# Kernel optimization log

Hardware: AMD Instinct MI355X
Metric: run time of the kernel (lower is better)

Reference implementation:

```python
import jax, jax.numpy as jnp
import numpy as np

NUM_HEADS = 16


def rotate_half(x):
    h = x.shape[-1] // 2
    return jnp.concatenate([-x[..., h:], x[..., :h]], axis=-1)


def setup_inputs() -> dict:
    key = jax.random.key(0)
    ks = jax.random.split(key, 8)
    S, dim, hd = 8192, 1280, 80
    n_seg = 8
    hidden_states = jax.random.normal(ks[0], (S, dim), dtype=jnp.float32)
    cu_seqlens = (jnp.arange(n_seg + 1, dtype=jnp.int32) * (S // n_seg))
    ang = jax.random.uniform(ks[1], (S, hd), dtype=jnp.float32) * (2.0 * np.pi)
    cos = jnp.cos(ang)
    sin = jnp.sin(ang)
    qkv_w = jax.random.normal(ks[2], (3 * dim, dim), dtype=jnp.float32) * (dim ** -0.5)
    qkv_b = jax.random.normal(ks[3], (3 * dim,), dtype=jnp.float32) * 0.02
    proj_w = jax.random.normal(ks[4], (dim, dim), dtype=jnp.float32) * (dim ** -0.5)
    proj_b = jax.random.normal(ks[5], (dim,), dtype=jnp.float32) * 0.02
    return {"hidden_states": hidden_states, "cu_seqlens": cu_seqlens,
            "cos": cos, "sin": sin, "qkv_w": qkv_w, "qkv_b": qkv_b,
            "proj_w": proj_w, "proj_b": proj_b}


def reference(hidden_states, cu_seqlens, cos, sin, qkv_w, qkv_b, proj_w, proj_b):
    S, dim = hidden_states.shape
    H = NUM_HEADS
    hd = dim // H
    scaling = hd ** -0.5

    # qkv projection: [S, 3*dim] -> [S, 3, H, hd]
    qkv = (hidden_states @ qkv_w.T + qkv_b).reshape(S, 3, H, hd)
    q, k, v = qkv[:, 0], qkv[:, 1], qkv[:, 2]  # each [S, H, hd]

    # RoPE in float32, cos/sin broadcast over heads
    c = cos[:, None, :].astype(jnp.float32)
    s = sin[:, None, :].astype(jnp.float32)
    qf, kf = q.astype(jnp.float32), k.astype(jnp.float32)
    q = (qf * c + rotate_half(qf) * s).astype(q.dtype)
    k = (kf * c + rotate_half(kf) * s).astype(k.dtype)

    # Block-diagonal varlen attention: equal-length segments -> batch dim
    lengths = np.diff(np.asarray(cu_seqlens))
    L = int(lengths[0])
    assert (lengths == L).all(), "reference assumes uniform segment lengths"
    B = lengths.shape[0]
    qb = q.reshape(B, L, H, hd)
    kb = k.reshape(B, L, H, hd)
    vb = v.reshape(B, L, H, hd)

    scores = jnp.einsum('blhd,bmhd->bhlm', qb, kb) * scaling
    probs = jax.nn.softmax(scores.astype(jnp.float32), axis=-1).astype(scores.dtype)
    out = jnp.einsum('bhlm,bmhd->blhd', probs, vb).reshape(S, dim)

    return out @ proj_w.T + proj_b
```

## Files before the change

### kernel.cpp

```cpp
#include <hip/hip_runtime.h>
#include <math.h>

typedef _Float16 f16;
typedef _Float16 half8 __attribute__((ext_vector_type(8)));
typedef _Float16 half4v __attribute__((ext_vector_type(4)));
typedef _Float16 half2v __attribute__((ext_vector_type(2)));
typedef float floatx4 __attribute__((ext_vector_type(4)));
typedef unsigned int u32;

#define AS1 __attribute__((address_space(1)))
#define AS3 __attribute__((address_space(3)))

__device__ __forceinline__ void stage16(f16* l, const f16* g) {
    __builtin_amdgcn_global_load_lds((const AS1 u32*)g, (AS3 u32*)l, 16, 0, 0);
}

__global__ __launch_bounds__(256) void cvt_f32_f16(const float* __restrict__ in,
                                                   f16* __restrict__ out, int n4) {
    int i = blockIdx.x * blockDim.x + threadIdx.x;
    if (i >= n4) return;
    float4 v = ((const float4*)in)[i];
    half4v h = {(f16)v.x, (f16)v.y, (f16)v.z, (f16)v.w};
    ((half4v*)out)[i] = h;
}

__global__ __launch_bounds__(256) void pack_w(const float* __restrict__ Wf,
                                              f16* __restrict__ Wp) {
    const int p = blockIdx.x * 256 + threadIdx.x;
    const int lane = p & 63;
    const int j = (p >> 6) & 3;
    const int sk = p >> 8;
    const int k0 = sk % 40;
    const int slab = sk / 40;
    const int row = slab * 64 + j * 16 + (lane & 15);
    const int col = k0 * 32 + (lane >> 4) * 8;
    const float* src = Wf + (size_t)row * 1280 + col;
    float4 a = *(const float4*)src;
    float4 b = *(const float4*)(src + 4);
    half8 h = {(f16)a.x, (f16)a.y, (f16)a.z, (f16)a.w,
               (f16)b.x, (f16)b.y, (f16)b.z, (f16)b.w};
    *(half8*)(Wp + (size_t)p * 8) = h;
}

constexpr int GK = 1280;
constexpr int KT = 20;

template <int MT>
__global__ __launch_bounds__(512, 2) void gemm_bp(const f16* __restrict__ A,
                                                  const f16* __restrict__ Bp,
                                                  const float* __restrict__ bias,
                                                  f16* __restrict__ outH,
                                                  float* __restrict__ outF,
                                                  int N, int NT) {
    constexpr int M_FR = MT / 32;
    constexpr int QE = MT * 32;
    __shared__ f16 sm[2][2][QE];
    const int t = threadIdx.x;
    const int lane = t & 63, w = t >> 6;
    const int wm = w >> 2, wn = w & 3;
    const int c16 = lane & 15, quad = lane >> 4;
    const int id = blockIdx.x;
    const int nx = (int)gridDim.x >> 3;
    const int gid = (id & 7) * nx + (id >> 3);
    const int bm = gid / NT, bn = gid - bm * NT;
    const f16* Ab = A + (size_t)bm * MT * GK;
    const f16* Bw = Bp + (size_t)(bn * 4 + wn) * (40 * 4 * 64 * 8) + lane * 8;

    floatx4 acc[M_FR][4] = {};
    half8 bfA[8], bfB[8];

    auto stageA = [&](int kt, int dst) {
#pragma unroll
        for (int ks = 0; ks < 2; ks++)
#pragma unroll
            for (int u = 0; u < MT / 128; u++) {
                const int c = t + u * 512;
                const int row = c >> 2;
                const int lc = ((c & 3) - (row >> 1)) & 3;
                stage16(&sm[dst][ks][0] + c * 8,
                        Ab + (size_t)row * GK + kt * 64 + ks * 32 + lc * 8);
            }
    };
    auto loadB = [&](int kt, half8(&bf)[8]) {
#pragma unroll
        for (int ks = 0; ks < 2; ks++)
#pragma unroll
            for (int j = 0; j < 4; j++)
                bf[ks * 4 + j] = *(const half8*)(Bw + (size_t)((kt * 2 + ks) * 4 + j) * 512);
    };
    auto compute = [&](int p, half8(&bf)[8]) {
#pragma unroll
        for (int ks = 0; ks < 2; ks++) {
            const f16* q = &sm[p][ks][0];
#pragma unroll
            for (int m = 0; m < M_FR; m++) {
                const int r = wm * (MT / 2) + m * 16 + c16;
                half8 a = *(const half8*)(q + r * 32 + (((quad + (r >> 1)) & 3) * 8));
#pragma unroll
                for (int n = 0; n < 4; n++)
                    acc[m][n] = __builtin_amdgcn_mfma_f32_16x16x32_f16(a, bf[ks * 4 + n],
                                                                       acc[m][n], 0, 0, 0);
            }
        }
    };
#define WAIT_STEADY()                                              \
    if constexpr (MT == 256) {                                     \
        asm volatile("s_waitcnt vmcnt(12)" ::: "memory");          \
    } else {                                                       \
        asm volatile("s_waitcnt vmcnt(10)" ::: "memory");          \
    }

    stageA(0, 0);
    loadB(0, bfA);
    asm volatile("s_waitcnt vmcnt(8)" ::: "memory");
    __builtin_amdgcn_s_barrier();

    for (int i = 0; i < 10; i++) {
        const int k0 = 2 * i;
        asm volatile("s_waitcnt lgkmcnt(0)" ::: "memory");
        __builtin_amdgcn_s_barrier();
        stageA(k0 + 1, 1);
        loadB(k0 + 1, bfB);
        WAIT_STEADY();
        __builtin_amdgcn_s_barrier();
        compute(0, bfA);
        asm volatile("s_waitcnt lgkmcnt(0)" ::: "memory");
        __builtin_amdgcn_s_barrier();
        if (i < 9) {
            stageA(k0 + 2, 0);
            loadB(k0 + 2, bfA);
            WAIT_STEADY();
        } else {
            asm volatile("s_waitcnt vmcnt(0)" ::: "memory");
        }
        __builtin_amdgcn_s_barrier();
        compute(1, bfB);
    }

    const int colBase = bn * 256 + wn * 64;
    const size_t rowBase = (size_t)bm * MT + wm * (MT / 2);
    float bv[4];
#pragma unroll
    for (int n = 0; n < 4; n++) bv[n] = bias[colBase + n * 16 + c16];
#pragma unroll
    for (int m = 0; m < M_FR; m++) {
#pragma unroll
        for (int r = 0; r < 4; r++) {
            const size_t row = rowBase + m * 16 + quad * 4 + r;
#pragma unroll
            for (int n = 0; n < 4; n++) {
                const int col = colBase + n * 16 + c16;
                const float v = acc[m][n][r] + bv[n];
                if (outH) outH[row * (size_t)N + col] = (f16)v;
                else      outF[row * (size_t)N + col] = v;
            }
        }
    }
}

#define QSCALE (0.11180339887498949f * 1.4426950408889634f)

__global__ __launch_bounds__(320) void rope_kernel(const f16* __restrict__ qkv,
                                                   const float* __restrict__ cosp,
                                                   const float* __restrict__ sinp,
                                                   f16* __restrict__ qb, f16* __restrict__ kb,
                                                   f16* __restrict__ vt) {
    constexpr int S = 8192;
    const int bs = blockIdx.x, h = blockIdx.y, t = threadIdx.x;
    const int sl = t / 5, g = t % 5;
    const int s = bs * 64 + sl;
    {
        const size_t base = (size_t)s * 3840 + h * 80 + g * 8;
        half8 qa = *(const half8*)(qkv + base);
        half8 qc = *(const half8*)(qkv + base + 40);
        half8 ka = *(const half8*)(qkv + base + 1280);
        half8 kc = *(const half8*)(qkv + base + 1320);
        const float* cp = cosp + (size_t)s * 80 + g * 8;
        const float* sp = sinp + (size_t)s * 80 + g * 8;
        half8 qo0, qo1, ko0, ko1;
#pragma unroll
        for (int j = 0; j < 8; j++) {
            float c0 = cp[j], c1 = cp[j + 40];
            float n0 = sp[j], n1 = sp[j + 40];
            float q0 = (float)qa[j], q1 = (float)qc[j];
            float k0 = (float)ka[j], k1 = (float)kc[j];
            qo0[j] = (f16)((q0 * c0 - q1 * n0) * QSCALE);
            qo1[j] = (f16)((q1 * c1 + q0 * n1) * QSCALE);
            ko0[j] = (f16)(k0 * c0 - k1 * n0);
            ko1[j] = (f16)(k1 * c1 + k0 * n1);
        }
        const size_t ob = ((size_t)h * S + s) * 96 + g * 8;
        *(half8*)(qb + ob)      = qo0;
        *(half8*)(qb + ob + 40) = qo1;
        *(half8*)(kb + ob)      = ko0;
        *(half8*)(kb + ob + 40) = ko1;
        if (g < 2) {
            half8 qp = {}, kp = {};
            if (g == 0) { qp[0] = (f16)(-8.0f); kp[0] = (f16)(1.0f); }
            const size_t pb = ((size_t)h * S + s) * 96 + 80 + g * 8;
            *(half8*)(qb + pb) = qp;
            *(half8*)(kb + pb) = kp;
        }
    }
    __shared__ f16 vls[64][81];
    for (int j = t; j < 64 * 80; j += 320) {
        int s2 = j / 80, d = j % 80;
        vls[s2][d] = qkv[((size_t)(bs * 64 + s2)) * 3840 + 2560 + h * 80 + d];
    }
    __syncthreads();
    for (int j = t; j < 64 * 80; j += 320) {
        int d = j >> 6, s2 = j & 63;
        vt[((size_t)(h * 80 + d)) * S + bs * 64 + s2] = vls[s2][d];
    }
}

__global__ __launch_bounds__(256, 2) void attn_kernel(const f16* __restrict__ qb,
                                                      const f16* __restrict__ kb,
                                                      const f16* __restrict__ vt,
                                                      const int* __restrict__ cu,
                                                      f16* __restrict__ out) {
    constexpr int S = 8192;
    __shared__ f16 Ks[2][64 * 96];
    __shared__ f16 Ps[256 * 72];
    const int t = threadIdx.x, lane = t & 63, w = t >> 6;
    const int c16 = lane & 15, quad = lane >> 4;
    const int id = blockIdx.x;
    const int pair = id & 127;
    const int qt = id >> 7;
    const int h = pair & 15, z = pair >> 4;
    const int s0 = cu[z];

    half8 qf[4][3];
#pragma unroll
    for (int qt2 = 0; qt2 < 4; qt2++)
#pragma unroll
        for (int ks = 0; ks < 3; ks++)
            qf[qt2][ks] = *(const half8*)(qb + ((size_t)h * S + s0 + qt * 256 + w * 64 + qt2 * 16 + c16) * 96 + ks * 32 + quad * 8);

    const f16 ov = (c16 == 0) ? (f16)1.f : (f16)0.f;
    const half8 onesf = {ov, ov, ov, ov, ov, ov, ov, ov};

    const int sR = t >> 2;
    const int sK = ((t & 3) - (sR >> 1)) & 3;

    {
        const f16* Kg = kb + ((size_t)h * S + s0) * 96;
#pragma unroll
        for (int j = 0; j < 3; j++)
            stage16(&Ks[0][0] + (j * 256 + t) * 8, Kg + (size_t)sR * 96 + j * 32 + sK * 8);
    }
    __syncthreads();

    floatx4 o[6][4] = {};

    for (int kv = 0; kv < 16; kv++) {
        if (kv < 15) {
            const f16* Kg = kb + ((size_t)h * S + s0 + (kv + 1) * 64) * 96;
            f16* Kd = &Ks[(kv + 1) & 1][0];
#pragma unroll
            for (int j = 0; j < 3; j++)
                stage16(Kd + (j * 256 + t) * 8, Kg + (size_t)sR * 96 + j * 32 + sK * 8);
        }
        const f16* Kc = &Ks[kv & 1][0];
        floatx4 sc[4][4] = {};
#pragma unroll
        for (int ks = 0; ks < 3; ks++) {
            half8 kf[4];
#pragma unroll
            for (int mt = 0; mt < 4; mt++) {
                const int row = mt * 16 + c16;
                kf[mt] = *(const half8*)(Kc + (ks * 256 + 4 * row + ((quad + (row >> 1)) & 3)) * 8);
            }
#pragma unroll
            for (int qt2 = 0; qt2 < 4; qt2++)
#pragma unroll
                for (int mt = 0; mt < 4; mt++)
                    sc[mt][qt2] = __builtin_amdgcn_mfma_f32_16x16x32_f16(kf[mt], qf[qt2][ks], sc[mt][qt2], 0, 0, 0);
        }
#pragma unroll
        for (int qt2 = 0; qt2 < 4; qt2++) {
            const int q = w * 64 + qt2 * 16 + c16;
#pragma unroll
            for (int mt = 0; mt < 4; mt++) {
                half4v pv;
#pragma unroll
                for (int r = 0; r < 4; r++)
                    pv[r] = (f16)__builtin_amdgcn_exp2f(sc[mt][qt2][r]);
                *(half4v*)(Ps + q * 72 + mt * 16 + quad * 4) = pv;
            }
        }
#pragma unroll
        for (int ks = 0; ks < 2; ks++) {
            const f16* Vg = vt + (size_t)h * 80 * S + s0 + kv * 64 + ks * 32;
            half8 vf[5];
#pragma unroll
            for (int dt = 0; dt < 5; dt++)
                vf[dt] = *(const half8*)(Vg + (size_t)(dt * 16 + c16) * S + quad * 8);
#pragma unroll
            for (int qt2 = 0; qt2 < 4; qt2++) {
                const int q = w * 64 + qt2 * 16 + c16;
                half8 pf = *(const half8*)(Ps + q * 72 + ks * 32 + quad * 8);
#pragma unroll
                for (int dt = 0; dt < 5; dt++)
                    o[dt][qt2] = __builtin_amdgcn_mfma_f32_16x16x32_f16(vf[dt], pf, o[dt][qt2], 0, 0, 0);
                o[5][qt2] = __builtin_amdgcn_mfma_f32_16x16x32_f16(onesf, pf, o[5][qt2], 0, 0, 0);
            }
        }
        __syncthreads();
    }
#pragma unroll
    for (int qt2 = 0; qt2 < 4; qt2++) {
        const float l = __shfl(o[5][qt2][0], c16);
        const float inv = 1.f / l;
        const size_t srow = (size_t)s0 + qt * 256 + w * 64 + qt2 * 16 + c16;
#pragma unroll
        for (int dt = 0; dt < 5; dt++)
#pragma unroll
            for (int rp = 0; rp < 2; rp++) {
                half2v hv = {(f16)(o[dt][qt2][rp * 2] * inv), (f16)(o[dt][qt2][rp * 2 + 1] * inv)};
                *(half2v*)(out + srow * 1280 + h * 80 + dt * 16 + quad * 4 + rp * 2) = hv;
            }
    }
}

extern "C" void kernel_launch(void* const* d_in, const int* in_sizes, int n_in,
                              void* d_out, int out_size, void* d_ws, size_t ws_size,
                              hipStream_t stream) {
    const float* hidden = (const float*)d_in[0];
    const int* cu       = (const int*)d_in[1];
    const float* cosp   = (const float*)d_in[2];
    const float* sinp   = (const float*)d_in[3];
    const float* qkv_w  = (const float*)d_in[4];
    const float* qkv_b  = (const float*)d_in[5];
    const float* proj_w = (const float*)d_in[6];
    const float* proj_b = (const float*)d_in[7];
    float* out = (float*)d_out;

    constexpr size_t S = 8192, DIM = 1280, N3 = 3840;
    f16* A16   = (f16*)d_ws;
    f16* WP16  = A16 + S * DIM;
    f16* PP16  = WP16 + N3 * DIM;
    f16* QKV16 = PP16 + DIM * DIM;
    f16* QB    = QKV16 + S * N3;
    f16* KB    = QB + (size_t)16 * S * 96;
    f16* VT    = KB + (size_t)16 * S * 96;
    f16* AT16  = A16;

    {
        int n4 = (int)(S * DIM / 4);
        cvt_f32_f16<<<(n4 + 255) / 256, 256, 0, stream>>>(hidden, A16, n4);
    }
    pack_w<<<(int)(N3 * DIM / 8 / 256), 256, 0, stream>>>(qkv_w, WP16);
    pack_w<<<(int)(DIM * DIM / 8 / 256), 256, 0, stream>>>(proj_w, PP16);
    gemm_bp<256><<<32 * 15, 512, 0, stream>>>(A16, WP16, qkv_b, QKV16, nullptr, 3840, 15);
    rope_kernel<<<dim3(128, 16), 320, 0, stream>>>(QKV16, cosp, sinp, QB, KB, VT);
    attn_kernel<<<512, 256, 0, stream>>>(QB, KB, VT, cu, A16);
    gemm_bp<128><<<64 * 5, 512, 0, stream>>>(AT16, PP16, proj_b, nullptr, out, 1280, 5);
}
```

Before: 375.8 us.

## Fuse prep kernels, switch GEMMs to 128x128 tiles, vectorize V staging

Merges the hidden-state conversion and both weight packing kernels into a single prep launch to cut launch overhead. Replaces the templated 512-thread GEMM (256x256 or 128x256 tiles) with a 256-thread 128x128-tile GEMM, which quadruples the grid for the QKV projection and doubles it for the output projection. This gives more blocks per CU and better tail balance, at the cost of less operand reuse per tile. The rope kernel's V transpose staging now loads 8 halves per global read instead of one.

```diff
diff --git a/kernel.cpp b/kernel.cpp
--- a/kernel.cpp
+++ b/kernel.cpp
@@ -15,18 +15,8 @@
     __builtin_amdgcn_global_load_lds((const AS1 u32*)g, (AS3 u32*)l, 16, 0, 0);
 }
 
-__global__ __launch_bounds__(256) void cvt_f32_f16(const float* __restrict__ in,
-                                                   f16* __restrict__ out, int n4) {
-    int i = blockIdx.x * blockDim.x + threadIdx.x;
-    if (i >= n4) return;
-    float4 v = ((const float4*)in)[i];
-    half4v h = {(f16)v.x, (f16)v.y, (f16)v.z, (f16)v.w};
-    ((half4v*)out)[i] = h;
-}
-
-__global__ __launch_bounds__(256) void pack_w(const float* __restrict__ Wf,
-                                              f16* __restrict__ Wp) {
-    const int p = blockIdx.x * 256 + threadIdx.x;
+__device__ __forceinline__ void pack_body(const float* __restrict__ Wf,
+                                          f16* __restrict__ Wp, int p) {
     const int lane = p & 63;
     const int j = (p >> 6) & 3;
     const int sk = p >> 8;
@@ -42,39 +32,54 @@
     *(half8*)(Wp + (size_t)p * 8) = h;
 }
 
+__global__ __launch_bounds__(256) void prep_kernel(const float* __restrict__ hidden,
+                                                   f16* __restrict__ A16,
+                                                   const float* __restrict__ qkv_w,
+                                                   f16* __restrict__ WP16,
+                                                   const float* __restrict__ proj_w,
+                                                   f16* __restrict__ PP16) {
+    const int b = blockIdx.x;
+    if (b < 10240) {
+        const int i = b * 256 + threadIdx.x;
+        float4 v = ((const float4*)hidden)[i];
+        half4v h = {(f16)v.x, (f16)v.y, (f16)v.z, (f16)v.w};
+        ((half4v*)A16)[i] = h;
+    } else if (b < 12640) {
+        pack_body(qkv_w, WP16, (b - 10240) * 256 + threadIdx.x);
+    } else {
+        pack_body(proj_w, PP16, (b - 12640) * 256 + threadIdx.x);
+    }
+}
+
 constexpr int GK = 1280;
-constexpr int KT = 20;
-
-template <int MT>
-__global__ __launch_bounds__(512, 2) void gemm_bp(const f16* __restrict__ A,
+
+__global__ __launch_bounds__(256, 2) void gemm128(const f16* __restrict__ A,
                                                   const f16* __restrict__ Bp,
                                                   const float* __restrict__ bias,
                                                   f16* __restrict__ outH,
                                                   float* __restrict__ outF,
                                                   int N, int NT) {
-    constexpr int M_FR = MT / 32;
-    constexpr int QE = MT * 32;
-    __shared__ f16 sm[2][2][QE];
+    __shared__ f16 sm[2][2][128 * 32];
     const int t = threadIdx.x;
     const int lane = t & 63, w = t >> 6;
-    const int wm = w >> 2, wn = w & 3;
+    const int wm = w & 1, wn = w >> 1;
     const int c16 = lane & 15, quad = lane >> 4;
     const int id = blockIdx.x;
     const int nx = (int)gridDim.x >> 3;
     const int gid = (id & 7) * nx + (id >> 3);
     const int bm = gid / NT, bn = gid - bm * NT;
-    const f16* Ab = A + (size_t)bm * MT * GK;
-    const f16* Bw = Bp + (size_t)(bn * 4 + wn) * (40 * 4 * 64 * 8) + lane * 8;
-
-    floatx4 acc[M_FR][4] = {};
+    const f16* Ab = A + (size_t)bm * 128 * GK;
+    const f16* Bw = Bp + (size_t)(bn * 2 + wn) * (40 * 4 * 64 * 8) + lane * 8;
+
+    floatx4 acc[4][4] = {};
     half8 bfA[8], bfB[8];
 
     auto stageA = [&](int kt, int dst) {
 #pragma unroll
         for (int ks = 0; ks < 2; ks++)
 #pragma unroll
-            for (int u = 0; u < MT / 128; u++) {
-                const int c = t + u * 512;
+            for (int u = 0; u < 2; u++) {
+                const int c = t + u * 256;
                 const int row = c >> 2;
                 const int lc = ((c & 3) - (row >> 1)) & 3;
                 stage16(&sm[dst][ks][0] + c * 8,
@@ -93,8 +98,8 @@
         for (int ks = 0; ks < 2; ks++) {
             const f16* q = &sm[p][ks][0];
 #pragma unroll
-            for (int m = 0; m < M_FR; m++) {
-                const int r = wm * (MT / 2) + m * 16 + c16;
+            for (int m = 0; m < 4; m++) {
+                const int r = wm * 64 + m * 16 + c16;
                 half8 a = *(const half8*)(q + r * 32 + (((quad + (r >> 1)) & 3) * 8));
 #pragma unroll
                 for (int n = 0; n < 4; n++)
@@ -103,12 +108,6 @@
             }
         }
     };
-#define WAIT_STEADY()                                              \
-    if constexpr (MT == 256) {                                     \
-        asm volatile("s_waitcnt vmcnt(12)" ::: "memory");          \
-    } else {                                                       \
-        asm volatile("s_waitcnt vmcnt(10)" ::: "memory");          \
-    }
 
     stageA(0, 0);
     loadB(0, bfA);
@@ -121,7 +120,7 @@
         __builtin_amdgcn_s_barrier();
         stageA(k0 + 1, 1);
         loadB(k0 + 1, bfB);
-        WAIT_STEADY();
+        asm volatile("s_waitcnt vmcnt(12)" ::: "memory");
         __builtin_amdgcn_s_barrier();
         compute(0, bfA);
         asm volatile("s_waitcnt lgkmcnt(0)" ::: "memory");
@@ -129,7 +128,7 @@
         if (i < 9) {
             stageA(k0 + 2, 0);
             loadB(k0 + 2, bfA);
-            WAIT_STEADY();
+            asm volatile("s_waitcnt vmcnt(12)" ::: "memory");
         } else {
             asm volatile("s_waitcnt vmcnt(0)" ::: "memory");
         }
@@ -137,13 +136,13 @@
         compute(1, bfB);
     }
 
-    const int colBase = bn * 256 + wn * 64;
-    const size_t rowBase = (size_t)bm * MT + wm * (MT / 2);
+    const int colBase = bn * 128 + wn * 64;
+    const size_t rowBase = (size_t)bm * 128 + wm * 64;
     float bv[4];
 #pragma unroll
     for (int n = 0; n < 4; n++) bv[n] = bias[colBase + n * 16 + c16];
 #pragma unroll
-    for (int m = 0; m < M_FR; m++) {
+    for (int m = 0; m < 4; m++) {
 #pragma unroll
         for (int r = 0; r < 4; r++) {
             const size_t row = rowBase + m * 16 + quad * 4 + r;
@@ -203,9 +202,11 @@
         }
     }
     __shared__ f16 vls[64][81];
-    for (int j = t; j < 64 * 80; j += 320) {
-        int s2 = j / 80, d = j % 80;
-        vls[s2][d] = qkv[((size_t)(bs * 64 + s2)) * 3840 + 2560 + h * 80 + d];
+    for (int j = t; j < 640; j += 320) {
+        const int s2 = j / 10, gg = j - s2 * 10;
+        half8 v = *(const half8*)(qkv + ((size_t)(bs * 64 + s2)) * 3840 + 2560 + h * 80 + gg * 8);
+#pragma unroll
+        for (int i = 0; i < 8; i++) vls[s2][gg * 8 + i] = v[i];
     }
     __syncthreads();
     for (int j = t; j < 64 * 80; j += 320) {
@@ -346,14 +347,9 @@
     f16* VT    = KB + (size_t)16 * S * 96;
     f16* AT16  = A16;
 
-    {
-        int n4 = (int)(S * DIM / 4);
-        cvt_f32_f16<<<(n4 + 255) / 256, 256, 0, stream>>>(hidden, A16, n4);
-    }
-    pack_w<<<(int)(N3 * DIM / 8 / 256), 256, 0, stream>>>(qkv_w, WP16);
-    pack_w<<<(int)(DIM * DIM / 8 / 256), 256, 0, stream>>>(proj_w, PP16);
-    gemm_bp<256><<<32 * 15, 512, 0, stream>>>(A16, WP16, qkv_b, QKV16, nullptr, 3840, 15);
+    prep_kernel<<<13440, 256, 0, stream>>>(hidden, A16, qkv_w, WP16, proj_w, PP16);
+    gemm128<<<64 * 30, 256, 0, stream>>>(A16, WP16, qkv_b, QKV16, nullptr, 3840, 30);
     rope_kernel<<<dim3(128, 16), 320, 0, stream>>>(QKV16, cosp, sinp, QB, KB, VT);
     attn_kernel<<<512, 256, 0, stream>>>(QB, KB, VT, cu, A16);
-    gemm_bp<128><<<64 * 5, 512, 0, stream>>>(AT16, PP16, proj_b, nullptr, out, 1280, 5);
-}
+    gemm128<<<64 * 10, 256, 0, stream>>>(AT16, PP16, proj_b, nullptr, out, 1280, 10);
+}
```

New measurement: 358.1 us. -4.7%, faster.
